# Kernel tuning notes

Hardware: AMD Instinct MI355X
Metric: run time of the kernel (lower is better)

The kernel has to match this reference:

```python
import jax, jax.numpy as jnp
import numpy as np

D_MODEL = 1024
N_HEADS = 16
NUM_PATTERN = 32
HEAD_DIM = D_MODEL // N_HEADS  # d_keys = d_values = 64


def sparsemax(z):
    # z: [..., S]; Euclidean projection of z onto the probability simplex
    S = z.shape[-1]
    z_sorted = -jnp.sort(-z, axis=-1)                       # descending
    cum = jnp.cumsum(z_sorted, axis=-1)
    k = jnp.arange(1, S + 1, dtype=z.dtype)
    support = (1.0 + k * z_sorted) > cum                    # [..., S] bool
    k_sup = jnp.sum(support, axis=-1, keepdims=True)        # int, size of support
    cum_sel = jnp.take_along_axis(cum, k_sup - 1, axis=-1)
    tau = (cum_sel - 1.0) / k_sup.astype(z.dtype)
    return jnp.maximum(z - tau, 0.0)


def setup_inputs() -> dict:
    key = jax.random.key(0)
    ks = jax.random.split(key, 10)
    s = 1.0 / np.sqrt(D_MODEL)
    inp = {
        "query": jax.random.normal(ks[0], (8, 4096, D_MODEL), dtype=jnp.float32),
        "key_param": jax.random.normal(ks[1], (1, NUM_PATTERN, D_MODEL), dtype=jnp.float32),
        "Wq": jax.random.normal(ks[2], (D_MODEL, N_HEADS * HEAD_DIM), dtype=jnp.float32) * s,
        "bq": jnp.zeros((N_HEADS * HEAD_DIM,), dtype=jnp.float32),
        "Wk": jax.random.normal(ks[3], (D_MODEL, N_HEADS * HEAD_DIM), dtype=jnp.float32) * s,
        "bk": jnp.zeros((N_HEADS * HEAD_DIM,), dtype=jnp.float32),
        "Wv": jax.random.normal(ks[4], (N_HEADS * HEAD_DIM, N_HEADS * HEAD_DIM), dtype=jnp.float32) * s,
        "bv": jnp.zeros((N_HEADS * HEAD_DIM,), dtype=jnp.float32),
        "Wo": jax.random.normal(ks[5], (N_HEADS * HEAD_DIM, D_MODEL), dtype=jnp.float32) * s,
        "bo": jnp.zeros((D_MODEL,), dtype=jnp.float32),
    }
    return inp


def reference(query, key_param, Wq, bq, Wk, bk, Wv, bv, Wo, bo):
    B, L, _ = query.shape
    S = key_param.shape[1]
    H, E = N_HEADS, HEAD_DIM
    D = HEAD_DIM

    k = jnp.broadcast_to(key_param, (B, S, D_MODEL))         # repeat over batch
    queries = (query @ Wq + bq).reshape(B, L, H, E)
    keys_flat = k @ Wk + bk                                  # [B, S, H*E]
    values = (keys_flat @ Wv + bv).reshape(B, S, H, D)
    keys = keys_flat.reshape(B, S, H, E)

    scale = 1.0 / np.sqrt(E)
    scores = jnp.einsum("blhe,bshe->bhls", queries, keys)    # [B, H, L, S]
    A = sparsemax(scale * scores)                            # sparse normalization over S
    out = jnp.einsum("bhls,bshd->blhd", A, values)           # [B, L, H, D]

    # mix=True: transpose(2,1) then view(B, L, -1) on contiguous data
    out = jnp.transpose(out, (0, 2, 1, 3)).reshape(B, L, H * D)
    return out @ Wo + bo
```

## Files before the change

kernel.cpp:

```cpp
#include <hip/hip_runtime.h>

typedef unsigned short u16;
typedef __attribute__((ext_vector_type(8))) short short8;
typedef __attribute__((ext_vector_type(4))) float v4f;

__device__ __forceinline__ float b2f(u16 u) {
  union { unsigned int i; float f; } v; v.i = ((unsigned int)u) << 16; return v.f;
}
__device__ __forceinline__ u16 f2b(float f) {
  unsigned int x = __float_as_uint(f);
  x += 0x7fffu + ((x >> 16) & 1u);
  return (u16)(x >> 16);
}
__device__ __forceinline__ float ldin(const void* p, size_t i, int f32) {
  return f32 ? ((const float*)p)[i] : b2f(((const u16*)p)[i]);
}

#define LDSW 40

__global__ void sniff_k(const void* __restrict__ q, int* __restrict__ flag) {
  __shared__ int cnt;
  if (threadIdx.x == 0) cnt = 0;
  __syncthreads();
  const u16* p = (const u16*)q;
  int w = 0;
  for (int i = threadIdx.x; i < 1024; i += 256) {
    u16 u = p[i];
    int e = (u >> 7) & 0xFF;
    if (u != 0 && u != 0x8000 && (e >= 0xC0 || e < 0x40)) w++;
  }
  atomicAdd(&cnt, w);
  __syncthreads();
  if (threadIdx.x == 0) *flag = (cnt >= 32) ? 1 : 0;
}

__global__ void kv_zero(float* __restrict__ Kf, float* __restrict__ Vf) {
  int i = blockIdx.x * 256 + threadIdx.x;
  Kf[i] = 0.f;
  Vf[i] = 0.f;
}

__global__ void gemm_skinny_atomic(const void* __restrict__ A, const void* __restrict__ W,
                                   const void* __restrict__ bias, float* __restrict__ C,
                                   const int* __restrict__ flag, int a_f32_always) {
  const int f32 = *flag;
  const int af = a_f32_always ? 1 : f32;
  const int t = blockIdx.x * 256 + threadIdx.x;
  const int kb = blockIdx.y;
  const int s = t >> 10, j = t & 1023;
  const int d0 = kb * 128;
  float acc = 0.f;
#pragma unroll 16
  for (int d = d0; d < d0 + 128; ++d)
    acc += ldin(A, (size_t)s * 1024 + d, af) * ldin(W, (size_t)d * 1024 + j, f32);
  if (kb == 0) acc += ldin(bias, j, f32);
  atomicAdd(&C[t], acc);
}

__global__ void kernel_K(const void* __restrict__ kp, const void* __restrict__ Wk,
                         const void* __restrict__ bk, float* __restrict__ Kf,
                         const int* __restrict__ flag) {
  const int f32 = *flag;
  int t = blockIdx.x * 256 + threadIdx.x;
  int s = t >> 10, j = t & 1023;
  float acc = 0.f;
#pragma unroll 8
  for (int d = 0; d < 1024; ++d)
    acc += ldin(kp, (size_t)s * 1024 + d, f32) * ldin(Wk, (size_t)d * 1024 + j, f32);
  Kf[t] = acc + ldin(bk, j, f32);
}

__global__ void kernel_V(const float* __restrict__ Kf, const void* __restrict__ Wv,
                         const void* __restrict__ bv, float* __restrict__ Vf,
                         const int* __restrict__ flag) {
  const int f32 = *flag;
  int t = blockIdx.x * 256 + threadIdx.x;
  int s = t >> 10, j = t & 1023;
  const float* kr = Kf + (size_t)s * 1024;
  float acc = 0.f;
#pragma unroll 8
  for (int d = 0; d < 1024; ++d) acc += kr[d] * ldin(Wv, (size_t)d * 1024 + j, f32);
  Vf[t] = acc + ldin(bv, j, f32);
}

__global__ void __launch_bounds__(256) kernel_M2(
    const float* __restrict__ Kf, const void* __restrict__ Wq,
    const void* __restrict__ bq, u16* __restrict__ Mt,
    float* __restrict__ bias_s, const int* __restrict__ flag) {
  const int f32 = *flag;
  const int blk = blockIdx.x;
  const int h = blk >> 4, dg = blk & 15;
  const int t = threadIdx.x;
  const int d = dg * 64 + (t & 63);
  const int sb = (t >> 6) * 8;
  __shared__ float ks2[64][32];
  for (int i = t; i < 2048; i += 256) {
    int s = i & 31, e = i >> 5;
    ks2[e][s] = Kf[(size_t)s * 1024 + h * 64 + e] * 0.125f;
  }
  __syncthreads();
  v4f a0 = {0.f, 0.f, 0.f, 0.f}, a1 = {0.f, 0.f, 0.f, 0.f};
  const size_t base = (size_t)d * 1024 + h * 64;
  for (int e0 = 0; e0 < 64; e0 += 8) {
    float wq[8];
    if (f32) {
      const float* W = (const float*)Wq;
      v4f v0 = *(const v4f*)(W + base + e0);
      v4f v1 = *(const v4f*)(W + base + e0 + 4);
#pragma unroll
      for (int q = 0; q < 4; ++q) { wq[q] = v0[q]; wq[4 + q] = v1[q]; }
    } else {
      const u16* W = (const u16*)Wq;
      union { uint4 v; u16 w[8]; } tv __attribute__((aligned(16)));
      tv.v = *(const uint4*)(W + base + e0);
#pragma unroll
      for (int q = 0; q < 8; ++q) wq[q] = b2f(tv.w[q]);
    }
#pragma unroll
    for (int e = 0; e < 8; ++e) {
      float w = wq[e];
      v4f k0 = *(const v4f*)&ks2[e0 + e][sb];
      v4f k1 = *(const v4f*)&ks2[e0 + e][sb + 4];
      a0 += w * k0;
      a1 += w * k1;
    }
  }
#pragma unroll
  for (int r = 0; r < 4; ++r) {
    Mt[(size_t)(h * 32 + sb + r) * 1024 + d]     = f2b(a0[r]);
    Mt[(size_t)(h * 32 + sb + 4 + r) * 1024 + d] = f2b(a1[r]);
  }
  if (dg == 0 && t < 32) {
    float a = 0.f;
    for (int e = 0; e < 64; ++e) a += ldin(bq, h * 64 + e, f32) * ks2[e][t];
    bias_s[h * 32 + t] = a;
  }
}

__global__ void kernel_N2(const float* __restrict__ Vf, const void* __restrict__ Wo,
                          u16* __restrict__ N2t, const int* __restrict__ flag) {
  const int f32 = *flag;
  int blk = blockIdx.x;
  int h = blk >> 6, r = (blk >> 2) & 15, jb = blk & 3;
  int tid = threadIdx.x;
  int j = jb * 256 + tid;
  __shared__ float vsl[2048];
  for (int i = tid; i < 2048; i += 256) {
    int s = i >> 6, d = i & 63;
    vsl[i] = Vf[(size_t)s * 1024 + h * 64 + d];
  }
  __syncthreads();
  float acc[32];
#pragma unroll
  for (int s = 0; s < 32; ++s) acc[s] = 0.f;
  for (int d = 0; d < 64; ++d) {
    float w = ldin(Wo, (size_t)(r * 64 + d) * 1024 + j, f32);
#pragma unroll
    for (int s = 0; s < 32; ++s) acc[s] += vsl[s * 64 + d] * w;
  }
  union { u16 o[32]; uint4 v[4]; } ou __attribute__((aligned(16)));
#pragma unroll
  for (int s = 0; s < 32; ++s) ou.o[s] = f2b(acc[s]);
  uint4* dst = (uint4*)(N2t + ((size_t)(h * 1024 + j)) * 512 + r * 32);
#pragma unroll
  for (int i = 0; i < 4; ++i) dst[i] = ou.v[i];
}

__global__ void kernel_bo(const void* __restrict__ bo, float* __restrict__ bo_f,
                          const int* __restrict__ flag) {
  const int f32 = *flag;
  int i = blockIdx.x * 256 + threadIdx.x;
  if (i < 1024) bo_f[i] = ldin(bo, i, f32);
}

__global__ void gemm_scores(const void* __restrict__ A, const u16* __restrict__ B,
                            const float* __restrict__ bias, u16* __restrict__ Z2,
                            const int* __restrict__ flag) {
  const int f32 = *flag;
  const int K = 1024;
  __shared__ u16 As[128 * LDSW] __attribute__((aligned(16)));
  __shared__ u16 Bs[128 * LDSW] __attribute__((aligned(16)));
  const int tid = threadIdx.x;
  const int wave = tid >> 6;
  const int lane = tid & 63;
  const int quad = lane >> 4;
  const int l16 = lane & 15;
  const int m0 = blockIdx.y * 128;
  const int n0 = blockIdx.x * 128;
  const int wm = (wave >> 1) * 64;
  const int wn = (wave & 1) * 64;

  v4f acc[4][4] = {};

  const int idx0 = tid, idx1 = 256 + tid;
  const int r0 = idx0 >> 2, c0 = (idx0 & 3) * 8;
  const int r1 = idx1 >> 2, c1 = (idx1 & 3) * 8;
  const u16* Bb = B + (size_t)n0 * K;

  for (int k0 = 0; k0 < K; k0 += 32) {
    size_t offA0 = (size_t)(m0 + r0) * K + k0 + c0;
    size_t offA1 = (size_t)(m0 + r1) * K + k0 + c1;
    if (!f32) {
      *(uint4*)&As[r0 * LDSW + c0] = *(const uint4*)((const u16*)A + offA0);
      *(uint4*)&As[r1 * LDSW + c1] = *(const uint4*)((const u16*)A + offA1);
    } else {
      const float* fA = (const float*)A;
      v4f a0 = *(const v4f*)(fA + offA0);
      v4f a1 = *(const v4f*)(fA + offA0 + 4);
      v4f a2 = *(const v4f*)(fA + offA1);
      v4f a3 = *(const v4f*)(fA + offA1 + 4);
      union { uint4 v; u16 w[8]; } t0 __attribute__((aligned(16)));
      union { uint4 v; u16 w[8]; } t1 __attribute__((aligned(16)));
#pragma unroll
      for (int e = 0; e < 4; ++e) { t0.w[e] = f2b(a0[e]); t0.w[e + 4] = f2b(a1[e]); }
#pragma unroll
      for (int e = 0; e < 4; ++e) { t1.w[e] = f2b(a2[e]); t1.w[e + 4] = f2b(a3[e]); }
      *(uint4*)&As[r0 * LDSW + c0] = t0.v;
      *(uint4*)&As[r1 * LDSW + c1] = t1.v;
    }
    *(uint4*)&Bs[r0 * LDSW + c0] = *(const uint4*)(Bb + (size_t)r0 * K + k0 + c0);
    *(uint4*)&Bs[r1 * LDSW + c1] = *(const uint4*)(Bb + (size_t)r1 * K + k0 + c1);
    __syncthreads();
    short8 af[4], bf[4];
#pragma unroll
    for (int i = 0; i < 4; ++i)
      af[i] = *(const short8*)&As[(wm + i * 16 + l16) * LDSW + quad * 8];
#pragma unroll
    for (int i = 0; i < 4; ++i)
      bf[i] = *(const short8*)&Bs[(wn + i * 16 + l16) * LDSW + quad * 8];
#pragma unroll
    for (int mi = 0; mi < 4; ++mi)
#pragma unroll
      for (int ni = 0; ni < 4; ++ni)
        acc[mi][ni] = __builtin_amdgcn_mfma_f32_16x16x32_bf16(af[mi], bf[ni], acc[mi][ni], 0, 0, 0);
    __syncthreads();
  }

#pragma unroll
  for (int ni = 0; ni < 4; ++ni) {
    const int col = n0 + wn + ni * 16 + l16;
    const float bcol = bias[col];
    const int h = col >> 5, s = col & 31;
#pragma unroll
    for (int mi = 0; mi < 4; ++mi) {
      const int rbase = m0 + wm + mi * 16 + quad * 4;
#pragma unroll
      for (int rr = 0; rr < 4; ++rr) {
        const int rw = rbase + rr;
        const size_t addr = (size_t)h * 1048576 + (size_t)(rw >> 4) * 512 + (rw & 15) * 32 + s;
        Z2[addr] = f2b(acc[mi][ni][rr] + bcol);
      }
    }
  }
}

__global__ void sparsemax_k(u16* __restrict__ Z) {
  int t = blockIdx.x * 256 + threadIdx.x;
  u16* zp = Z + (size_t)t * 32;
  union { uint4 v[4]; u16 w[32]; } raw __attribute__((aligned(16)));
  const uint4* rp4 = (const uint4*)zp;
#pragma unroll
  for (int i = 0; i < 4; ++i) raw.v[i] = rp4[i];
  float z[32], zs[32];
#pragma unroll
  for (int i = 0; i < 32; ++i) { z[i] = b2f(raw.w[i]); zs[i] = z[i]; }
#pragma unroll
  for (int kk = 2; kk <= 32; kk <<= 1) {
#pragma unroll
    for (int j = kk >> 1; j > 0; j >>= 1) {
#pragma unroll
      for (int i = 0; i < 32; ++i) {
        int ij = i ^ j;
        if (ij > i) {
          bool up = ((i & kk) == 0);
          float a = zs[i], b = zs[ij];
          float hi = fmaxf(a, b), lo = fminf(a, b);
          zs[i]  = up ? hi : lo;
          zs[ij] = up ? lo : hi;
        }
      }
    }
  }
  float cum = 0.f, cumsel = 0.f;
  int ksup = 1;
#pragma unroll
  for (int i = 0; i < 32; ++i) {
    cum += zs[i];
    if (1.f + (float)(i + 1) * zs[i] > cum) { ksup = i + 1; cumsel = cum; }
  }
  float tau = (cumsel - 1.f) / (float)ksup;
  union { u16 o[32]; uint4 v[4]; } ou __attribute__((aligned(16)));
#pragma unroll
  for (int i = 0; i < 32; ++i) ou.o[i] = f2b(fmaxf(z[i] - tau, 0.f));
  uint4* op = (uint4*)zp;
#pragma unroll
  for (int i = 0; i < 4; ++i) op[i] = ou.v[i];
}

__global__ void gemm_out(const u16* __restrict__ Z2, const u16* __restrict__ N2t,
                         const float* __restrict__ bias, void* __restrict__ out,
                         const int* __restrict__ flag) {
  const int f32 = *flag;
  const int K = 512;
  const int h = blockIdx.z;
  __shared__ u16 As[128 * LDSW] __attribute__((aligned(16)));
  __shared__ u16 Bs[128 * LDSW] __attribute__((aligned(16)));
  const int tid = threadIdx.x;
  const int wave = tid >> 6;
  const int lane = tid & 63;
  const int quad = lane >> 4;
  const int l16 = lane & 15;
  const int m0 = blockIdx.y * 128;
  const int n0 = blockIdx.x * 128;
  const int wm = (wave >> 1) * 64;
  const int wn = (wave & 1) * 64;

  v4f acc[4][4] = {};

  const u16* Ab = Z2 + (size_t)h * 2048 * 512 + (size_t)m0 * K;
  const u16* Bb = N2t + (size_t)h * 1024 * 512 + (size_t)n0 * K;
  const int idx0 = tid, idx1 = 256 + tid;
  const int r0 = idx0 >> 2, c0 = (idx0 & 3) * 8;
  const int r1 = idx1 >> 2, c1 = (idx1 & 3) * 8;

  for (int k0 = 0; k0 < K; k0 += 32) {
    *(uint4*)&As[r0 * LDSW + c0] = *(const uint4*)(Ab + (size_t)r0 * K + k0 + c0);
    *(uint4*)&As[r1 * LDSW + c1] = *(const uint4*)(Ab + (size_t)r1 * K + k0 + c1);
    *(uint4*)&Bs[r0 * LDSW + c0] = *(const uint4*)(Bb + (size_t)r0 * K + k0 + c0);
    *(uint4*)&Bs[r1 * LDSW + c1] = *(const uint4*)(Bb + (size_t)r1 * K + k0 + c1);
    __syncthreads();
    short8 af[4], bf[4];
#pragma unroll
    for (int i = 0; i < 4; ++i)
      af[i] = *(const short8*)&As[(wm + i * 16 + l16) * LDSW + quad * 8];
#pragma unroll
    for (int i = 0; i < 4; ++i)
      bf[i] = *(const short8*)&Bs[(wn + i * 16 + l16) * LDSW + quad * 8];
#pragma unroll
    for (int mi = 0; mi < 4; ++mi)
#pragma unroll
      for (int ni = 0; ni < 4; ++ni)
        acc[mi][ni] = __builtin_amdgcn_mfma_f32_16x16x32_bf16(af[mi], bf[ni], acc[mi][ni], 0, 0, 0);
    __syncthreads();
  }

  float bv4[4];
#pragma unroll
  for (int ni = 0; ni < 4; ++ni) bv4[ni] = bias[n0 + wn + ni * 16 + l16];
#pragma unroll
  for (int mi = 0; mi < 4; ++mi) {
    const int rl = m0 + wm + mi * 16 + quad * 4;
#pragma unroll
    for (int rr = 0; rr < 4; ++rr) {
      const int rlr = rl + rr;
      const int orow = (rlr >> 8) * 4096 + h * 256 + (rlr & 255);
#pragma unroll
      for (int ni = 0; ni < 4; ++ni) {
        const int col = n0 + wn + ni * 16 + l16;
        const float v = acc[mi][ni][rr] + bv4[ni];
        const size_t oi = (size_t)orow * 1024 + col;
        if (f32) ((float*)out)[oi] = v;
        else     ((u16*)out)[oi] = f2b(v);
      }
    }
  }
}

__global__ void __launch_bounds__(256) fused_fallback(
    const void* __restrict__ query, const u16* __restrict__ Mt,
    const float* __restrict__ bias_s, const u16* __restrict__ N2t,
    const float* __restrict__ bo_f, void* __restrict__ out,
    const int* __restrict__ flag) {
  const int f32 = *flag;
  __shared__ float sc[256 * 32];
  __shared__ u16 qch[256 * 72];
  __shared__ u16 mh[32 * 64];
  const int t = threadIdx.x;
  const int bb = blockIdx.x;
  const int b = bb >> 4, atile = bb & 15;
  const int l0 = atile * 256;
  const size_t qbase = ((size_t)b * 4096 + l0) * 1024;

  for (int h = 0; h < 16; ++h) {
    float acc32[32];
#pragma unroll
    for (int s = 0; s < 32; ++s) acc32[s] = bias_s[h * 32 + s];
    for (int d0 = 0; d0 < 1024; d0 += 64) {
      __syncthreads();
#pragma unroll
      for (int i = 0; i < 8; ++i) {
        int f4 = t + i * 256;
        int row = f4 >> 3, c8 = f4 & 7;
        size_t off = qbase + (size_t)row * 1024 + d0 + c8 * 8;
        if (!f32) {
          *(uint4*)&qch[row * 72 + c8 * 8] = *(const uint4*)((const u16*)query + off);
        } else {
          union { uint4 v; u16 w[8]; } tq __attribute__((aligned(16)));
#pragma unroll
          for (int e = 0; e < 8; ++e) tq.w[e] = f2b(((const float*)query)[off + e]);
          *(uint4*)&qch[row * 72 + c8 * 8] = tq.v;
        }
      }
      { int row = t >> 3, c8 = t & 7;
        *(uint4*)&mh[row * 64 + c8 * 8] =
            *(const uint4*)(Mt + (size_t)(h * 32 + row) * 1024 + d0 + c8 * 8); }
      __syncthreads();
      float qrow[64];
#pragma unroll
      for (int c = 0; c < 64; ++c) qrow[c] = b2f(qch[t * 72 + c]);
#pragma unroll 4
      for (int s = 0; s < 32; ++s) {
        float a = 0.f;
#pragma unroll
        for (int c = 0; c < 64; ++c) a += qrow[c] * b2f(mh[s * 64 + c]);
        acc32[s] += a;
      }
    }
    float zs[32];
#pragma unroll
    for (int i = 0; i < 32; ++i) zs[i] = acc32[i];
#pragma unroll
    for (int kk = 2; kk <= 32; kk <<= 1) {
#pragma unroll
      for (int j = kk >> 1; j > 0; j >>= 1) {
#pragma unroll
        for (int i = 0; i < 32; ++i) {
          int ij = i ^ j;
          if (ij > i) {
            bool up = ((i & kk) == 0);
            float a = zs[i], bq_ = zs[ij];
            float hi = fmaxf(a, bq_), lo = fminf(a, bq_);
            zs[i]  = up ? hi : lo;
            zs[ij] = up ? lo : hi;
          }
        }
      }
    }
    float cum = 0.f, cumsel = 0.f;
    int ksup = 1;
#pragma unroll
    for (int i = 0; i < 32; ++i) {
      cum += zs[i];
      if (1.f + (float)(i + 1) * zs[i] > cum) { ksup = i + 1; cumsel = cum; }
    }
    float tau = (cumsel - 1.f) / (float)ksup;
#pragma unroll
    for (int s = 0; s < 32; ++s) sc[t * 32 + s] = fmaxf(acc32[s] - tau, 0.f);
    __syncthreads();
    for (int jj = 0; jj < 4; ++jj) {
      int j = t + jj * 256;
      const u16* nrow = N2t + ((size_t)h * 1024 + j) * 512;
      float acc16[16];
#pragma unroll
      for (int a = 0; a < 16; ++a) acc16[a] = 0.f;
      for (int k0 = 0; k0 < 512; k0 += 8) {
        union { uint4 v; u16 w[8]; } nv __attribute__((aligned(16)));
        nv.v = *(const uint4*)(nrow + k0);
#pragma unroll
        for (int kk = 0; kk < 8; ++kk) {
          float nf = b2f(nv.w[kk]);
#pragma unroll
          for (int a = 0; a < 16; ++a) acc16[a] += sc[a * 512 + k0 + kk] * nf;
        }
      }
      float bj = bo_f[j];
#pragma unroll
      for (int a = 0; a < 16; ++a) {
        int orow = b * 4096 + h * 256 + atile * 16 + a;
        size_t oi = (size_t)orow * 1024 + j;
        float v = acc16[a] + bj;
        if (f32) ((float*)out)[oi] = v;
        else     ((u16*)out)[oi] = f2b(v);
      }
    }
    __syncthreads();
  }
}

__global__ void zero_out(void* __restrict__ out, int n, const int* __restrict__ flag) {
  const int f32 = *flag;
  int i = blockIdx.x * 256 + threadIdx.x;
  if (i < n) { if (f32) ((float*)out)[i] = 0.f; else ((u16*)out)[i] = 0; }
}

extern "C" void kernel_launch(void* const* d_in, const int* in_sizes, int n_in,
                              void* d_out, int out_size, void* d_ws, size_t ws_size,
                              hipStream_t stream) {
  const void* query = d_in[0];
  const void* kp    = d_in[1];
  const void* Wq    = d_in[2];
  const void* bq    = d_in[3];
  const void* Wk    = d_in[4];
  const void* bk    = d_in[5];
  const void* Wv    = d_in[6];
  const void* bv    = d_in[7];
  const void* Wo    = d_in[8];
  const void* bo    = d_in[9];

  char* ws = (char*)d_ws;
  int*   flag   = (int*)(ws);
  float* Kf     = (float*)(ws + (64 << 10));
  float* Vf     = (float*)(ws + (192 << 10));
  float* bias_s = (float*)(ws + (320 << 10));
  float* bo_f   = (float*)(ws + (324 << 10));
  u16*   Mt     = (u16*)(ws + (1 << 20));
  u16*   N2t    = (u16*)(ws + (2 << 20));
  u16*   Z2     = (u16*)(ws + (18 << 20));

  const size_t WS_FAST = (size_t)(18 << 20) + 33554432;
  const size_t WS_FALL = (size_t)(18 << 20);

  sniff_k<<<1, 256, 0, stream>>>(query, flag);

  if (ws_size >= WS_FAST) {
    kv_zero<<<128, 256, 0, stream>>>(Kf, Vf);
    gemm_skinny_atomic<<<dim3(128, 8), 256, 0, stream>>>(kp, Wk, bk, Kf, flag, 0);
    gemm_skinny_atomic<<<dim3(128, 8), 256, 0, stream>>>(Kf, Wv, bv, Vf, flag, 1);
    kernel_M2<<<256, 256, 0, stream>>>(Kf, Wq, bq, Mt, bias_s, flag);
    kernel_N2<<<1024, 256, 0, stream>>>(Vf, Wo, N2t, flag);
    kernel_bo<<<4, 256, 0, stream>>>(bo, bo_f, flag);
    gemm_scores<<<dim3(512 / 128, 32768 / 128), 256, 0, stream>>>(query, Mt, bias_s, Z2, flag);
    sparsemax_k<<<2048, 256, 0, stream>>>(Z2);
    gemm_out<<<dim3(1024 / 128, 2048 / 128, 16), 256, 0, stream>>>(Z2, N2t, bo_f, d_out, flag);
  } else if (ws_size >= WS_FALL) {
    kernel_K<<<128, 256, 0, stream>>>(kp, Wk, bk, Kf, flag);
    kernel_V<<<128, 256, 0, stream>>>(Kf, Wv, bv, Vf, flag);
    kernel_M2<<<256, 256, 0, stream>>>(Kf, Wq, bq, Mt, bias_s, flag);
    kernel_N2<<<1024, 256, 0, stream>>>(Vf, Wo, N2t, flag);
    kernel_bo<<<4, 256, 0, stream>>>(bo, bo_f, flag);
    fused_fallback<<<128, 256, 0, stream>>>(query, Mt, bias_s, N2t, bo_f, d_out, flag);
  } else {
    zero_out<<<(out_size + 255) / 256, 256, 0, stream>>>(d_out, out_size, flag);
  }
}
```

Baseline: 464.9 us.

## Widen score and output GEMM tiles to 128x512 with 512-thread blocks

```diff
diff --git a/kernel.cpp b/kernel.cpp
--- a/kernel.cpp
+++ b/kernel.cpp
@@ -173,72 +173,65 @@
   if (i < 1024) bo_f[i] = ldin(bo, i, f32);
 }
 
-__global__ void gemm_scores(const void* __restrict__ A, const u16* __restrict__ B,
-                            const float* __restrict__ bias, u16* __restrict__ Z2,
-                            const int* __restrict__ flag) {
+__global__ void __launch_bounds__(512, 1) gemm_scores_wide(
+    const void* __restrict__ A, const u16* __restrict__ B,
+    const float* __restrict__ bias, u16* __restrict__ Z2,
+    const int* __restrict__ flag) {
   const int f32 = *flag;
   const int K = 1024;
   __shared__ u16 As[128 * LDSW] __attribute__((aligned(16)));
-  __shared__ u16 Bs[128 * LDSW] __attribute__((aligned(16)));
+  __shared__ u16 Bs[512 * LDSW] __attribute__((aligned(16)));
   const int tid = threadIdx.x;
   const int wave = tid >> 6;
   const int lane = tid & 63;
   const int quad = lane >> 4;
   const int l16 = lane & 15;
-  const int m0 = blockIdx.y * 128;
-  const int n0 = blockIdx.x * 128;
-  const int wm = (wave >> 1) * 64;
-  const int wn = (wave & 1) * 64;
-
-  v4f acc[4][4] = {};
-
-  const int idx0 = tid, idx1 = 256 + tid;
-  const int r0 = idx0 >> 2, c0 = (idx0 & 3) * 8;
-  const int r1 = idx1 >> 2, c1 = (idx1 & 3) * 8;
-  const u16* Bb = B + (size_t)n0 * K;
+  const int m0 = blockIdx.x * 128;
+  const int wm = (wave >> 2) * 64;
+  const int wn = (wave & 3) * 128;
+
+  v4f acc[4][8] = {};
+
+  const int ra = tid >> 2, ca = (tid & 3) * 8;
 
   for (int k0 = 0; k0 < K; k0 += 32) {
-    size_t offA0 = (size_t)(m0 + r0) * K + k0 + c0;
-    size_t offA1 = (size_t)(m0 + r1) * K + k0 + c1;
+    size_t offA = (size_t)(m0 + ra) * K + k0 + ca;
     if (!f32) {
-      *(uint4*)&As[r0 * LDSW + c0] = *(const uint4*)((const u16*)A + offA0);
-      *(uint4*)&As[r1 * LDSW + c1] = *(const uint4*)((const u16*)A + offA1);
+      *(uint4*)&As[ra * LDSW + ca] = *(const uint4*)((const u16*)A + offA);
     } else {
       const float* fA = (const float*)A;
-      v4f a0 = *(const v4f*)(fA + offA0);
-      v4f a1 = *(const v4f*)(fA + offA0 + 4);
-      v4f a2 = *(const v4f*)(fA + offA1);
-      v4f a3 = *(const v4f*)(fA + offA1 + 4);
+      v4f a0 = *(const v4f*)(fA + offA);
+      v4f a1 = *(const v4f*)(fA + offA + 4);
       union { uint4 v; u16 w[8]; } t0 __attribute__((aligned(16)));
-      union { uint4 v; u16 w[8]; } t1 __attribute__((aligned(16)));
 #pragma unroll
       for (int e = 0; e < 4; ++e) { t0.w[e] = f2b(a0[e]); t0.w[e + 4] = f2b(a1[e]); }
-#pragma unroll
-      for (int e = 0; e < 4; ++e) { t1.w[e] = f2b(a2[e]); t1.w[e + 4] = f2b(a3[e]); }
-      *(uint4*)&As[r0 * LDSW + c0] = t0.v;
-      *(uint4*)&As[r1 * LDSW + c1] = t1.v;
-    }
-    *(uint4*)&Bs[r0 * LDSW + c0] = *(const uint4*)(Bb + (size_t)r0 * K + k0 + c0);
-    *(uint4*)&Bs[r1 * LDSW + c1] = *(const uint4*)(Bb + (size_t)r1 * K + k0 + c1);
+      *(uint4*)&As[ra * LDSW + ca] = t0.v;
+    }
+#pragma unroll
+    for (int p = 0; p < 4; ++p) {
+      int idx = tid + p * 512;
+      int rb = idx >> 2, cb = (idx & 3) * 8;
+      *(uint4*)&Bs[rb * LDSW + cb] = *(const uint4*)(B + (size_t)rb * K + k0 + cb);
+    }
     __syncthreads();
-    short8 af[4], bf[4];
+    short8 af[4], bf[8];
 #pragma unroll
     for (int i = 0; i < 4; ++i)
       af[i] = *(const short8*)&As[(wm + i * 16 + l16) * LDSW + quad * 8];
 #pragma unroll
-    for (int i = 0; i < 4; ++i)
+    for (int i = 0; i < 8; ++i)
       bf[i] = *(const short8*)&Bs[(wn + i * 16 + l16) * LDSW + quad * 8];
 #pragma unroll
     for (int mi = 0; mi < 4; ++mi)
 #pragma unroll
-      for (int ni = 0; ni < 4; ++ni)
+      for (int ni = 0; ni < 8; ++ni)
         acc[mi][ni] = __builtin_amdgcn_mfma_f32_16x16x32_bf16(af[mi], bf[ni], acc[mi][ni], 0, 0, 0);
     __syncthreads();
   }
 
 #pragma unroll
-  for (int ni = 0; ni < 4; ++ni) {
-    const int col = n0 + wn + ni * 16 + l16;
+  for (int ni = 0; ni < 8; ++ni) {
+    const int col = wn + ni * 16 + l16;
     const float bcol = bias[col];
     const int h = col >> 5, s = col & 31;
 #pragma unroll
@@ -297,56 +290,58 @@
   for (int i = 0; i < 4; ++i) op[i] = ou.v[i];
 }
 
-__global__ void gemm_out(const u16* __restrict__ Z2, const u16* __restrict__ N2t,
-                         const float* __restrict__ bias, void* __restrict__ out,
-                         const int* __restrict__ flag) {
+__global__ void __launch_bounds__(512, 1) gemm_out_wide(
+    const u16* __restrict__ Z2, const u16* __restrict__ N2t,
+    const float* __restrict__ bias, void* __restrict__ out,
+    const int* __restrict__ flag) {
   const int f32 = *flag;
   const int K = 512;
   const int h = blockIdx.z;
   __shared__ u16 As[128 * LDSW] __attribute__((aligned(16)));
-  __shared__ u16 Bs[128 * LDSW] __attribute__((aligned(16)));
+  __shared__ u16 Bs[512 * LDSW] __attribute__((aligned(16)));
   const int tid = threadIdx.x;
   const int wave = tid >> 6;
   const int lane = tid & 63;
   const int quad = lane >> 4;
   const int l16 = lane & 15;
   const int m0 = blockIdx.y * 128;
-  const int n0 = blockIdx.x * 128;
-  const int wm = (wave >> 1) * 64;
-  const int wn = (wave & 1) * 64;
-
-  v4f acc[4][4] = {};
+  const int n0 = blockIdx.x * 512;
+  const int wm = (wave >> 2) * 64;
+  const int wn = (wave & 3) * 128;
+
+  v4f acc[4][8] = {};
 
   const u16* Ab = Z2 + (size_t)h * 2048 * 512 + (size_t)m0 * K;
   const u16* Bb = N2t + (size_t)h * 1024 * 512 + (size_t)n0 * K;
-  const int idx0 = tid, idx1 = 256 + tid;
-  const int r0 = idx0 >> 2, c0 = (idx0 & 3) * 8;
-  const int r1 = idx1 >> 2, c1 = (idx1 & 3) * 8;
+  const int ra = tid >> 2, ca = (tid & 3) * 8;
 
   for (int k0 = 0; k0 < K; k0 += 32) {
-    *(uint4*)&As[r0 * LDSW + c0] = *(const uint4*)(Ab + (size_t)r0 * K + k0 + c0);
-    *(uint4*)&As[r1 * LDSW + c1] = *(const uint4*)(Ab + (size_t)r1 * K + k0 + c1);
-    *(uint4*)&Bs[r0 * LDSW + c0] = *(const uint4*)(Bb + (size_t)r0 * K + k0 + c0);
-    *(uint4*)&Bs[r1 * LDSW + c1] = *(const uint4*)(Bb + (size_t)r1 * K + k0 + c1);
+    *(uint4*)&As[ra * LDSW + ca] = *(const uint4*)(Ab + (size_t)ra * K + k0 + ca);
+#pragma unroll
+    for (int p = 0; p < 4; ++p) {
+      int idx = tid + p * 512;
+      int rb = idx >> 2, cb = (idx & 3) * 8;
+      *(uint4*)&Bs[rb * LDSW + cb] = *(const uint4*)(Bb + (size_t)rb * K + k0 + cb);
+    }
     __syncthreads();
-    short8 af[4], bf[4];
+    short8 af[4], bf[8];
 #pragma unroll
     for (int i = 0; i < 4; ++i)
       af[i] = *(const short8*)&As[(wm + i * 16 + l16) * LDSW + quad * 8];
 #pragma unroll
-    for (int i = 0; i < 4; ++i)
+    for (int i = 0; i < 8; ++i)
       bf[i] = *(const short8*)&Bs[(wn + i * 16 + l16) * LDSW + quad * 8];
 #pragma unroll
     for (int mi = 0; mi < 4; ++mi)
 #pragma unroll
-      for (int ni = 0; ni < 4; ++ni)
+      for (int ni = 0; ni < 8; ++ni)
         acc[mi][ni] = __builtin_amdgcn_mfma_f32_16x16x32_bf16(af[mi], bf[ni], acc[mi][ni], 0, 0, 0);
     __syncthreads();
   }
 
-  float bv4[4];
-#pragma unroll
-  for (int ni = 0; ni < 4; ++ni) bv4[ni] = bias[n0 + wn + ni * 16 + l16];
+  float bv8[8];
+#pragma unroll
+  for (int ni = 0; ni < 8; ++ni) bv8[ni] = bias[n0 + wn + ni * 16 + l16];
 #pragma unroll
   for (int mi = 0; mi < 4; ++mi) {
     const int rl = m0 + wm + mi * 16 + quad * 4;
@@ -355,9 +350,9 @@
       const int rlr = rl + rr;
       const int orow = (rlr >> 8) * 4096 + h * 256 + (rlr & 255);
 #pragma unroll
-      for (int ni = 0; ni < 4; ++ni) {
+      for (int ni = 0; ni < 8; ++ni) {
         const int col = n0 + wn + ni * 16 + l16;
-        const float v = acc[mi][ni][rr] + bv4[ni];
+        const float v = acc[mi][ni][rr] + bv8[ni];
         const size_t oi = (size_t)orow * 1024 + col;
         if (f32) ((float*)out)[oi] = v;
         else     ((u16*)out)[oi] = f2b(v);
@@ -519,9 +514,9 @@
     kernel_M2<<<256, 256, 0, stream>>>(Kf, Wq, bq, Mt, bias_s, flag);
     kernel_N2<<<1024, 256, 0, stream>>>(Vf, Wo, N2t, flag);
     kernel_bo<<<4, 256, 0, stream>>>(bo, bo_f, flag);
-    gemm_scores<<<dim3(512 / 128, 32768 / 128), 256, 0, stream>>>(query, Mt, bias_s, Z2, flag);
+    gemm_scores_wide<<<256, 512, 0, stream>>>(query, Mt, bias_s, Z2, flag);
     sparsemax_k<<<2048, 256, 0, stream>>>(Z2);
-    gemm_out<<<dim3(1024 / 128, 2048 / 128, 16), 256, 0, stream>>>(Z2, N2t, bo_f, d_out, flag);
+    gemm_out_wide<<<dim3(2, 16, 16), 512, 0, stream>>>(Z2, N2t, bo_f, d_out, flag);
   } else if (ws_size >= WS_FALL) {
     kernel_K<<<128, 256, 0, stream>>>(kp, Wk, bk, Kf, flag);
     kernel_V<<<128, 256, 0, stream>>>(Kf, Wv, bv, Vf, flag);
```

After: 451.1 us. 3.0% less time.
